# Optimization experiments

Hardware: AMD Instinct MI355X
Metric: run time of the kernel (lower is better)

## Reference

```python
import jax, jax.numpy as jnp
import numpy as np

SHAPE = (2048, 2048, 3, 3)  # conv kernel gradient [out_c, in_c, kh, kw]


def setup_inputs() -> dict:
    key = jax.random.key(0)
    k1, k2 = jax.random.split(key)
    grad = jax.random.normal(k1, SHAPE, dtype=jnp.float32)
    residual = jax.random.normal(k2, SHAPE, dtype=jnp.float32) * 0.1  # accumulated momentum residual self.layers[name]
    momentum = jnp.float32(0.9)
    k = int(np.prod(SHAPE) * 0.1 / 100)
    return {"grad": grad, "residual": residual, "momentum": momentum, "k": k}


def reference(grad, residual, momentum, k):
    # current_layer = tensor + self.layers[name], flattened
    flat = (grad + residual).reshape(-1)
    # top-k by absolute value
    _, idx_unsorted = jax.lax.top_k(jnp.abs(flat), k)
    vals_unsorted = flat[idx_unsorted]
    # sort selected entries by (signed) value, as torch.argsort(top_values_unsorted)
    order = jnp.argsort(vals_unsorted)
    top_values = vals_unsorted[order]
    top_indices = idx_unsorted[order]

    gflat = grad.reshape(-1)
    # small_values_tensor = grad with top entries zeroed (put_ with zeros)
    small = gflat.at[top_indices].set(0.0)
    # residual: zero top entries, then accumulate momentum-weighted small gradients
    new_residual = residual.reshape(-1).at[top_indices].set(0.0) + small * momentum
    # construct_grads: zeros with top values scattered at top_indices
    sparse_grad = jnp.zeros_like(gflat).at[top_indices].set(top_values)

    return (top_indices,
            top_values,
            new_residual.reshape(grad.shape),
            sparse_grad.reshape(grad.shape))
```

## Files before the change

kernel.cpp:

```cpp
#include <hip/hip_runtime.h>

typedef unsigned int u32;
typedef unsigned long long u64;

#define CAND_MAX 131072u
#define MEMB_MAX 65536u
#define SORT_N   65536u

__device__ __forceinline__ u32 fkey32(u32 fb) {
  return (fb & 0x80000000u) ? ~fb : (fb | 0x80000000u);
}

__global__ void k_hist(const float4* __restrict__ g, const float4* __restrict__ r,
                       int n4, u32* __restrict__ hist) {
  __shared__ u32 lh[2048];
  for (int i = threadIdx.x; i < 2048; i += blockDim.x) lh[i] = 0;
  __syncthreads();
  int stride = gridDim.x * blockDim.x;
  for (int i = blockIdx.x * blockDim.x + threadIdx.x; i < n4; i += stride) {
    float4 a = g[i]; float4 b = r[i];
    u32 u0 = __float_as_uint(a.x + b.x) & 0x7fffffffu;
    u32 u1 = __float_as_uint(a.y + b.y) & 0x7fffffffu;
    u32 u2 = __float_as_uint(a.z + b.z) & 0x7fffffffu;
    u32 u3 = __float_as_uint(a.w + b.w) & 0x7fffffffu;
    atomicAdd(&lh[u0 >> 20], 1u);
    atomicAdd(&lh[u1 >> 20], 1u);
    atomicAdd(&lh[u2 >> 20], 1u);
    atomicAdd(&lh[u3 >> 20], 1u);
  }
  __syncthreads();
  for (int i = threadIdx.x; i < 2048; i += blockDim.x)
    if (lh[i]) atomicAdd(&hist[i], lh[i]);
}

__global__ void __launch_bounds__(1024) k_scan(const u32* __restrict__ hist,
                                               u32* __restrict__ ctrl, int k) {
  __shared__ u32 b0[2048], b1[2048];
  u32 t = threadIdx.x;
  b0[t] = hist[t]; b0[t + 1024] = hist[t + 1024];
  __syncthreads();
  u32* src = b0; u32* dst = b1;
  for (u32 off = 1; off < 2048; off <<= 1) {
    for (u32 i = t; i < 2048; i += 1024) {
      u32 v = src[i];
      if (i + off < 2048) v += src[i + off];
      dst[i] = v;
    }
    __syncthreads();
    u32* tmp = src; src = dst; dst = tmp;
  }
  u32 K = (u32)k;
  for (u32 i = t; i < 2048; i += 1024) {
    u32 cum = src[i];
    u32 nxt = (i + 1 < 2048) ? src[i + 1] : 0u;
    if (cum >= K && nxt < K) {
      ctrl[0] = i;
      ctrl[1] = nxt;
      ctrl[2] = K - nxt;
    }
  }
}

__global__ void k_main(const float4* __restrict__ g, const float4* __restrict__ r,
                       const float* __restrict__ momp,
                       float4* __restrict__ res4, float4* __restrict__ sp4,
                       u32* __restrict__ ctrl, u64* __restrict__ cand,
                       u64* __restrict__ memb, int n4) {
  float m = *momp;
  u32 B = ctrl[0];
  int stride = gridDim.x * blockDim.x;
  for (int i = blockIdx.x * blockDim.x + threadIdx.x; i < n4; i += stride) {
    float4 a = g[i]; float4 b = r[i];
    float4 ro, so;
    u32 base = (u32)i * 4u;
#define PROC(X, J, RO, SO) { \
    float c = a.X + b.X; \
    u32 cb = __float_as_uint(c); \
    u32 u = cb & 0x7fffffffu; \
    u32 bin = u >> 20; \
    float rv = b.X + m * a.X; float sv = 0.f; \
    if (bin >= B) { \
      u32 idx = base + J; \
      if (bin > B) { \
        rv = 0.f; sv = c; \
        u32 slot = atomicAdd(&ctrl[4], 1u); \
        if (slot < MEMB_MAX) memb[slot] = ((u64)fkey32(cb) << 32) | (u64)idx; \
      } else { \
        u32 slot = atomicAdd(&ctrl[3], 1u); \
        if (slot < CAND_MAX) cand[slot] = ((u64)u << 32) | (u64)(idx | (cb & 0x80000000u)); \
      } \
    } \
    RO = rv; SO = sv; }
    PROC(x, 0u, ro.x, so.x)
    PROC(y, 1u, ro.y, so.y)
    PROC(z, 2u, ro.z, so.z)
    PROC(w, 3u, ro.w, so.w)
#undef PROC
    res4[i] = ro;
    sp4[i] = so;
  }
}

__global__ void __launch_bounds__(1024) k_refine(u32* __restrict__ ctrl,
                                                 const u64* __restrict__ cand) {
  __shared__ u32 h[1024], h2[1024];
  __shared__ u32 tie[2048];
  __shared__ u32 res[4];
  __shared__ u32 nt;
  u32 t = threadIdx.x;
  u32 nc = ctrl[3]; if (nc > CAND_MAX) nc = CAND_MAX;
  u32 r = ctrl[2];
  u32 B12 = ctrl[0];

  h[t] = 0; if (t == 0) nt = 0;
  __syncthreads();
  for (u32 i = t; i < nc; i += 1024) {
    u32 u = (u32)(cand[i] >> 32);
    atomicAdd(&h[(u >> 10) & 1023u], 1u);
  }
  __syncthreads();
  u32* src = h; u32* dst = h2;
  for (u32 off = 1; off < 1024; off <<= 1) {
    u32 v = src[t] + ((t + off < 1024) ? src[t + off] : 0u);
    dst[t] = v;
    __syncthreads();
    u32* tmp = src; src = dst; dst = tmp;
  }
  {
    u32 cum = src[t];
    u32 nxt = (t + 1 < 1024) ? src[t + 1] : 0u;
    if (cum >= r && nxt < r) { res[0] = t; res[1] = nxt; }
  }
  __syncthreads();
  u32 B1 = res[0];
  u32 r1 = r - res[1];
  __syncthreads();

  h[t] = 0; h2[t] = 0;
  __syncthreads();
  for (u32 i = t; i < nc; i += 1024) {
    u32 u = (u32)(cand[i] >> 32);
    if (((u >> 10) & 1023u) == B1) atomicAdd(&h[u & 1023u], 1u);
  }
  __syncthreads();
  src = h; dst = h2;
  for (u32 off = 1; off < 1024; off <<= 1) {
    u32 v = src[t] + ((t + off < 1024) ? src[t + off] : 0u);
    dst[t] = v;
    __syncthreads();
    u32* tmp = src; src = dst; dst = tmp;
  }
  {
    u32 cum = src[t];
    u32 nxt = (t + 1 < 1024) ? src[t + 1] : 0u;
    if (cum >= r1 && nxt < r1) { res[2] = t; res[3] = nxt; }
  }
  __syncthreads();
  u32 B2 = res[2];
  u32 r2 = r1 - res[3];
  u32 T = (B12 << 20) | (B1 << 10) | B2;
  __syncthreads();

  for (u32 i = t; i < nc; i += 1024) {
    u64 e = cand[i];
    if ((u32)(e >> 32) == T) {
      u32 p = atomicAdd(&nt, 1u);
      if (p < 2048u) tie[p] = (u32)e & 0x7fffffffu;
    }
  }
  __syncthreads();
  u32 ntc = nt; if (ntc > 2048u) ntc = 2048u;
  for (u32 i = t; i < ntc; i += 1024) {
    u32 ti = tie[i];
    u32 rank = 0;
    for (u32 j = 0; j < ntc; j++) rank += (tie[j] < ti) ? 1u : 0u;
    if (rank == r2 - 1u) ctrl[6] = ti;
  }
  if (t == 0) ctrl[5] = T;
}

__global__ void k_patch(u32* __restrict__ ctrl, const u64* __restrict__ cand,
                        float* __restrict__ res_out, float* __restrict__ sp_out,
                        u64* __restrict__ memb) {
  u32 nc = ctrl[3]; if (nc > CAND_MAX) nc = CAND_MAX;
  u32 T = ctrl[5];
  u32 cut = ctrl[6];
  u32 stride = gridDim.x * blockDim.x;
  for (u32 i = blockIdx.x * blockDim.x + threadIdx.x; i < nc; i += stride) {
    u64 e = cand[i];
    u32 u = (u32)(e >> 32);
    u32 low = (u32)e;
    u32 idx = low & 0x7fffffffu;
    bool chosen = (u > T) || (u == T && idx <= cut);
    if (chosen) {
      u32 cb = u | (low & 0x80000000u);
      res_out[idx] = 0.f;
      sp_out[idx] = __uint_as_float(cb);
      u32 slot = atomicAdd(&ctrl[4], 1u);
      if (slot < MEMB_MAX) memb[slot] = ((u64)fkey32(cb) << 32) | (u64)idx;
    }
  }
}

__global__ void k_pad(u64* __restrict__ memb, int k) {
  int i = blockIdx.x * blockDim.x + threadIdx.x;
  if (i >= k && i < (int)SORT_N) memb[i] = ~0ull;
}

__global__ void __launch_bounds__(1024) k_blocal(u64* __restrict__ d) {
  __shared__ u64 s[8192];
  u32 base = blockIdx.x * 8192u;
  for (u32 i = threadIdx.x; i < 8192u; i += blockDim.x) s[i] = d[base + i];
  __syncthreads();
  for (u32 kk = 2; kk <= 8192u; kk <<= 1) {
    for (u32 jj = kk >> 1; jj > 0; jj >>= 1) {
      for (u32 t = threadIdx.x; t < 4096u; t += blockDim.x) {
        u32 i = 2u * t - (t & (jj - 1u));
        u32 l = i + jj;
        u64 x = s[i], y = s[l];
        bool up = (((base + i) & kk) == 0u);
        bool sw = up ? (x > y) : (y > x);
        if (sw) { s[i] = y; s[l] = x; }
      }
      __syncthreads();
    }
  }
  for (u32 i = threadIdx.x; i < 8192u; i += blockDim.x) d[base + i] = s[i];
}

__global__ void __launch_bounds__(1024) k_bstep(u64* __restrict__ d, u32 kk, u32 jj) {
  u32 t = blockIdx.x * blockDim.x + threadIdx.x;
  u32 i = 2u * t - (t & (jj - 1u));
  u32 l = i + jj;
  u64 x = d[i], y = d[l];
  bool up = ((i & kk) == 0u);
  bool sw = up ? (x > y) : (y > x);
  if (sw) { d[i] = y; d[l] = x; }
}

__global__ void __launch_bounds__(1024) k_bmerge(u64* __restrict__ d, u32 kk) {
  __shared__ u64 s[8192];
  u32 base = blockIdx.x * 8192u;
  for (u32 i = threadIdx.x; i < 8192u; i += blockDim.x) s[i] = d[base + i];
  __syncthreads();
  for (u32 jj = 4096u; jj > 0; jj >>= 1) {
    for (u32 t = threadIdx.x; t < 4096u; t += blockDim.x) {
      u32 i = 2u * t - (t & (jj - 1u));
      u32 l = i + jj;
      u64 x = s[i], y = s[l];
      bool up = (((base + i) & kk) == 0u);
      bool sw = up ? (x > y) : (y > x);
      if (sw) { s[i] = y; s[l] = x; }
    }
    __syncthreads();
  }
  for (u32 i = threadIdx.x; i < 8192u; i += blockDim.x) d[base + i] = s[i];
}

__global__ void k_write(const u64* __restrict__ memb, float* __restrict__ out, int k) {
  int i = blockIdx.x * blockDim.x + threadIdx.x;
  if (i >= k) return;
  u64 e = memb[i];
  u32 idx = (u32)e;
  u32 h = (u32)(e >> 32);
  u32 fb = (h & 0x80000000u) ? (h ^ 0x80000000u) : ~h;
  out[i] = (float)idx;
  out[k + i] = __uint_as_float(fb);
}

extern "C" void kernel_launch(void* const* d_in, const int* in_sizes, int n_in,
                              void* d_out, int out_size, void* d_ws, size_t ws_size,
                              hipStream_t stream) {
  const float* g   = (const float*)d_in[0];
  const float* r   = (const float*)d_in[1];
  const float* mom = (const float*)d_in[2];
  int n = in_sizes[0];
  int k = (out_size - 2 * n) / 2;
  int n4 = n / 4;

  float* out = (float*)d_out;
  float* res_out = out + 2 * (size_t)k;
  float* sp_out  = res_out + (size_t)n;

  unsigned char* ws = (unsigned char*)d_ws;
  u32* hist = (u32*)ws;
  u32* ctrl = (u32*)(ws + 8192);
  u64* cand = (u64*)(ws + 16384);
  u64* memb = (u64*)(ws + 16384 + (size_t)CAND_MAX * 8);

  hipMemsetAsync(ws, 0, 16384, stream);

  k_hist<<<2048, 256, 0, stream>>>((const float4*)g, (const float4*)r, n4, hist);
  k_scan<<<1, 1024, 0, stream>>>(hist, ctrl, k);
  k_main<<<2048, 256, 0, stream>>>((const float4*)g, (const float4*)r, mom,
                                   (float4*)res_out, (float4*)sp_out,
                                   ctrl, cand, memb, n4);
  k_refine<<<1, 1024, 0, stream>>>(ctrl, cand);
  k_patch<<<256, 256, 0, stream>>>(ctrl, cand, res_out, sp_out, memb);
  k_pad<<<SORT_N / 256, 256, 0, stream>>>(memb, k);

  k_blocal<<<SORT_N / 8192, 1024, 0, stream>>>(memb);
  for (u32 kk = 16384u; kk <= SORT_N; kk <<= 1) {
    for (u32 jj = kk >> 1; jj >= 8192u; jj >>= 1)
      k_bstep<<<SORT_N / 2048, 1024, 0, stream>>>(memb, kk, jj);
    k_bmerge<<<SORT_N / 8192, 1024, 0, stream>>>(memb, kk);
  }

  k_write<<<(SORT_N + 255) / 256, 256, 0, stream>>>(memb, out, k);
}
```

Measured before the change: 1.160 ms.

## Replace full histogram pass with sampled threshold and wave-aggregated candidate append

Drops the full-tensor histogram pass and instead builds the coarse histogram from a sparse sample (1024 float4 per 32768 chunk), picking a looser threshold that targets about 4k candidates. The main pass writes only the residual and appends all above-threshold entries to the candidate list using wave-level ballot aggregation rather than per-element atomics. Refinement now does three histogram levels over the candidates, and the sparse output is zeroed with a memset. This removes one full read of both inputs and most global atomic contention. The cost is a larger candidate buffer, an extra refine level, a memset over the sparse output, and a dependence on the sample being representative: if the sample underestimates, fewer than k entries may fall above the threshold.

```diff
diff --git a/kernel.cpp b/kernel.cpp
--- a/kernel.cpp
+++ b/kernel.cpp
@@ -3,41 +3,66 @@
 typedef unsigned int u32;
 typedef unsigned long long u64;
 
-#define CAND_MAX 131072u
-#define MEMB_MAX 65536u
-#define SORT_N   65536u
+#define SORT_N 65536u
+
+#define C_PT    0
+#define C_NC    16
+#define C_T     32
+#define C_CUT   33
+#define C_NM    48
 
 __device__ __forceinline__ u32 fkey32(u32 fb) {
   return (fb & 0x80000000u) ? ~fb : (fb | 0x80000000u);
 }
 
-__global__ void k_hist(const float4* __restrict__ g, const float4* __restrict__ r,
-                       int n4, u32* __restrict__ hist) {
+__device__ __forceinline__ u32 lane_id() {
+  return __builtin_amdgcn_mbcnt_hi(~0u, __builtin_amdgcn_mbcnt_lo(~0u, 0u));
+}
+
+__device__ __forceinline__ u32 wave_append(u32* ctr, bool pred) {
+  u64 mask = __ballot(pred);
+  if (mask == 0ull) return 0xffffffffu;
+  u32 lane = lane_id();
+  u32 slot = 0xffffffffu;
+  if (pred) {
+    u32 rank = (u32)__popcll(mask & ((1ull << lane) - 1ull));
+    int leader = __ffsll((unsigned long long)mask) - 1;
+    u32 base = 0;
+    if ((int)lane == leader) base = atomicAdd(ctr, (u32)__popcll(mask));
+    base = (u32)__shfl((int)base, leader, 64);
+    slot = base + rank;
+  }
+  return slot;
+}
+
+__global__ void __launch_bounds__(256) k_sample(const float4* __restrict__ g,
+                                                const float4* __restrict__ r,
+                                                u32* __restrict__ shist, int n4) {
   __shared__ u32 lh[2048];
-  for (int i = threadIdx.x; i < 2048; i += blockDim.x) lh[i] = 0;
-  __syncthreads();
-  int stride = gridDim.x * blockDim.x;
-  for (int i = blockIdx.x * blockDim.x + threadIdx.x; i < n4; i += stride) {
-    float4 a = g[i]; float4 b = r[i];
-    u32 u0 = __float_as_uint(a.x + b.x) & 0x7fffffffu;
-    u32 u1 = __float_as_uint(a.y + b.y) & 0x7fffffffu;
-    u32 u2 = __float_as_uint(a.z + b.z) & 0x7fffffffu;
-    u32 u3 = __float_as_uint(a.w + b.w) & 0x7fffffffu;
-    atomicAdd(&lh[u0 >> 20], 1u);
-    atomicAdd(&lh[u1 >> 20], 1u);
-    atomicAdd(&lh[u2 >> 20], 1u);
-    atomicAdd(&lh[u3 >> 20], 1u);
-  }
-  __syncthreads();
-  for (int i = threadIdx.x; i < 2048; i += blockDim.x)
-    if (lh[i]) atomicAdd(&hist[i], lh[i]);
-}
-
-__global__ void __launch_bounds__(1024) k_scan(const u32* __restrict__ hist,
-                                               u32* __restrict__ ctrl, int k) {
+  for (int i = threadIdx.x; i < 2048; i += 256) lh[i] = 0;
+  __syncthreads();
+  u32 base = blockIdx.x * 32768u;
+#pragma unroll
+  for (int j = 0; j < 4; j++) {
+    u32 i = base + threadIdx.x + (u32)j * 256u;
+    if ((int)i < n4) {
+      float4 a = g[i]; float4 b = r[i];
+      atomicAdd(&lh[(__float_as_uint(a.x + b.x) & 0x7fffffffu) >> 20], 1u);
+      atomicAdd(&lh[(__float_as_uint(a.y + b.y) & 0x7fffffffu) >> 20], 1u);
+      atomicAdd(&lh[(__float_as_uint(a.z + b.z) & 0x7fffffffu) >> 20], 1u);
+      atomicAdd(&lh[(__float_as_uint(a.w + b.w) & 0x7fffffffu) >> 20], 1u);
+    }
+  }
+  __syncthreads();
+  for (int i = threadIdx.x; i < 2048; i += 256)
+    if (lh[i]) atomicAdd(&shist[i], lh[i]);
+}
+
+__global__ void __launch_bounds__(1024) k_pick(const u32* __restrict__ shist,
+                                               u32* __restrict__ ctrl, u32 target) {
   __shared__ u32 b0[2048], b1[2048];
   u32 t = threadIdx.x;
-  b0[t] = hist[t]; b0[t + 1024] = hist[t + 1024];
+  b0[t] = shist[t]; b0[t + 1024] = shist[t + 1024];
   __syncthreads();
   u32* src = b0; u32* dst = b1;
   for (u32 off = 1; off < 2048; off <<= 1) {
@@ -49,79 +74,93 @@
     __syncthreads();
     u32* tmp = src; src = dst; dst = tmp;
   }
-  u32 K = (u32)k;
   for (u32 i = t; i < 2048; i += 1024) {
     u32 cum = src[i];
     u32 nxt = (i + 1 < 2048) ? src[i + 1] : 0u;
-    if (cum >= K && nxt < K) {
-      ctrl[0] = i;
-      ctrl[1] = nxt;
-      ctrl[2] = K - nxt;
-    }
-  }
-}
-
-__global__ void k_main(const float4* __restrict__ g, const float4* __restrict__ r,
-                       const float* __restrict__ momp,
-                       float4* __restrict__ res4, float4* __restrict__ sp4,
-                       u32* __restrict__ ctrl, u64* __restrict__ cand,
-                       u64* __restrict__ memb, int n4) {
-  float m = *momp;
-  u32 B = ctrl[0];
-  int stride = gridDim.x * blockDim.x;
-  for (int i = blockIdx.x * blockDim.x + threadIdx.x; i < n4; i += stride) {
-    float4 a = g[i]; float4 b = r[i];
-    float4 ro, so;
-    u32 base = (u32)i * 4u;
-#define PROC(X, J, RO, SO) { \
-    float c = a.X + b.X; \
-    u32 cb = __float_as_uint(c); \
+    if (cum >= target && nxt < target) ctrl[C_PT] = i;
+  }
+}
+
+__global__ void __launch_bounds__(256) k_main1(const float4* __restrict__ g,
+                                               const float4* __restrict__ r,
+                                               const float* __restrict__ momp,
+                                               float4* __restrict__ res4,
+                                               u32* __restrict__ ctrl,
+                                               u64* __restrict__ cand, u32 cap, int n4) {
+  int i = blockIdx.x * 256 + (int)threadIdx.x;
+  if (i >= n4) return;
+  float m = momp[0];
+  u32 PT = ctrl[C_PT];
+  float4 a = g[i];
+  float4 b = r[i];
+  float4 ro;
+  ro.x = b.x + m * a.x; ro.y = b.y + m * a.y;
+  ro.z = b.z + m * a.z; ro.w = b.w + m * a.w;
+  res4[i] = ro;
+  u32 base4 = (u32)i * 4u;
+  float cv0 = a.x + b.x, cv1 = a.y + b.y, cv2 = a.z + b.z, cv3 = a.w + b.w;
+#define COMPACT(CV, J) { \
+    u32 cb = __float_as_uint(CV); \
     u32 u = cb & 0x7fffffffu; \
-    u32 bin = u >> 20; \
-    float rv = b.X + m * a.X; float sv = 0.f; \
-    if (bin >= B) { \
-      u32 idx = base + J; \
-      if (bin > B) { \
-        rv = 0.f; sv = c; \
-        u32 slot = atomicAdd(&ctrl[4], 1u); \
-        if (slot < MEMB_MAX) memb[slot] = ((u64)fkey32(cb) << 32) | (u64)idx; \
-      } else { \
-        u32 slot = atomicAdd(&ctrl[3], 1u); \
-        if (slot < CAND_MAX) cand[slot] = ((u64)u << 32) | (u64)(idx | (cb & 0x80000000u)); \
-      } \
-    } \
-    RO = rv; SO = sv; }
-    PROC(x, 0u, ro.x, so.x)
-    PROC(y, 1u, ro.y, so.y)
-    PROC(z, 2u, ro.z, so.z)
-    PROC(w, 3u, ro.w, so.w)
-#undef PROC
-    res4[i] = ro;
-    sp4[i] = so;
-  }
+    bool pred = (u >> 20) >= PT; \
+    u32 slot = wave_append(&ctrl[C_NC], pred); \
+    if (pred && slot < cap) \
+      cand[slot] = ((u64)u << 32) | (u64)((base4 + J) | (cb & 0x80000000u)); \
+  }
+  COMPACT(cv0, 0u)
+  COMPACT(cv1, 1u)
+  COMPACT(cv2, 2u)
+  COMPACT(cv3, 3u)
+#undef COMPACT
 }
 
 __global__ void __launch_bounds__(1024) k_refine(u32* __restrict__ ctrl,
-                                                 const u64* __restrict__ cand) {
-  __shared__ u32 h[1024], h2[1024];
+                                                 const u64* __restrict__ cand,
+                                                 u32 cap, u32 K) {
+  __shared__ u32 h[2048], h2[2048];
+  __shared__ u32 res[8];
   __shared__ u32 tie[2048];
-  __shared__ u32 res[4];
   __shared__ u32 nt;
   u32 t = threadIdx.x;
-  u32 nc = ctrl[3]; if (nc > CAND_MAX) nc = CAND_MAX;
-  u32 r = ctrl[2];
-  u32 B12 = ctrl[0];
-
-  h[t] = 0; if (t == 0) nt = 0;
+  u32 nc = ctrl[C_NC]; if (nc > cap) nc = cap;
+
+  h[t] = 0; h[t + 1024] = 0;
+  if (t == 0) nt = 0;
+  __syncthreads();
+  for (u32 i = t; i < nc; i += 1024)
+    atomicAdd(&h[(u32)(cand[i] >> 52)], 1u);
+  __syncthreads();
+  u32* src = h; u32* dst = h2;
+  for (u32 off = 1; off < 2048; off <<= 1) {
+    for (u32 i = t; i < 2048; i += 1024) {
+      u32 v = src[i];
+      if (i + off < 2048) v += src[i + off];
+      dst[i] = v;
+    }
+    __syncthreads();
+    u32* tmp = src; src = dst; dst = tmp;
+  }
+  for (u32 i = t; i < 2048; i += 1024) {
+    u32 cum = src[i];
+    u32 nxt = (i + 1 < 2048) ? src[i + 1] : 0u;
+    if (cum >= K && nxt < K) { res[0] = i; res[1] = nxt; }
+  }
+  __syncthreads();
+  u32 B0 = res[0];
+  u32 r0 = K - res[1];
+  __syncthreads();
+
+  h[t] = 0;
   __syncthreads();
   for (u32 i = t; i < nc; i += 1024) {
     u32 u = (u32)(cand[i] >> 32);
-    atomicAdd(&h[(u >> 10) & 1023u], 1u);
-  }
-  __syncthreads();
-  u32* src = h; u32* dst = h2;
+    if ((u >> 20) == B0) atomicAdd(&h[(u >> 10) & 1023u], 1u);
+  }
+  __syncthreads();
+  src = h; dst = h2;
   for (u32 off = 1; off < 1024; off <<= 1) {
-    u32 v = src[t] + ((t + off < 1024) ? src[t + off] : 0u);
+    u32 v = src[t];
+    if (t + off < 1024) v += src[t + off];
     dst[t] = v;
     __syncthreads();
     u32* tmp = src; src = dst; dst = tmp;
@@ -129,23 +168,25 @@
   {
     u32 cum = src[t];
     u32 nxt = (t + 1 < 1024) ? src[t + 1] : 0u;
-    if (cum >= r && nxt < r) { res[0] = t; res[1] = nxt; }
-  }
-  __syncthreads();
-  u32 B1 = res[0];
-  u32 r1 = r - res[1];
-  __syncthreads();
-
-  h[t] = 0; h2[t] = 0;
+    if (cum >= r0 && nxt < r0) { res[2] = t; res[3] = nxt; }
+  }
+  __syncthreads();
+  u32 B1 = res[2];
+  u32 r1 = r0 - res[3];
+  u32 hi21 = (B0 << 10) | B1;
+  __syncthreads();
+
+  h[t] = 0;
   __syncthreads();
   for (u32 i = t; i < nc; i += 1024) {
     u32 u = (u32)(cand[i] >> 32);
-    if (((u >> 10) & 1023u) == B1) atomicAdd(&h[u & 1023u], 1u);
+    if ((u >> 10) == hi21) atomicAdd(&h[u & 1023u], 1u);
   }
   __syncthreads();
   src = h; dst = h2;
   for (u32 off = 1; off < 1024; off <<= 1) {
-    u32 v = src[t] + ((t + off < 1024) ? src[t + off] : 0u);
+    u32 v = src[t];
+    if (t + off < 1024) v += src[t + off];
     dst[t] = v;
     __syncthreads();
     u32* tmp = src; src = dst; dst = tmp;
@@ -153,12 +194,12 @@
   {
     u32 cum = src[t];
     u32 nxt = (t + 1 < 1024) ? src[t + 1] : 0u;
-    if (cum >= r1 && nxt < r1) { res[2] = t; res[3] = nxt; }
-  }
-  __syncthreads();
-  u32 B2 = res[2];
-  u32 r2 = r1 - res[3];
-  u32 T = (B12 << 20) | (B1 << 10) | B2;
+    if (cum >= r1 && nxt < r1) { res[4] = t; res[5] = nxt; }
+  }
+  __syncthreads();
+  u32 B2 = res[4];
+  u32 r2 = r1 - res[5];
+  u32 T = (hi21 << 10) | B2;
   __syncthreads();
 
   for (u32 i = t; i < nc; i += 1024) {
@@ -174,30 +215,38 @@
     u32 ti = tie[i];
     u32 rank = 0;
     for (u32 j = 0; j < ntc; j++) rank += (tie[j] < ti) ? 1u : 0u;
-    if (rank == r2 - 1u) ctrl[6] = ti;
-  }
-  if (t == 0) ctrl[5] = T;
-}
-
-__global__ void k_patch(u32* __restrict__ ctrl, const u64* __restrict__ cand,
-                        float* __restrict__ res_out, float* __restrict__ sp_out,
-                        u64* __restrict__ memb) {
-  u32 nc = ctrl[3]; if (nc > CAND_MAX) nc = CAND_MAX;
-  u32 T = ctrl[5];
-  u32 cut = ctrl[6];
-  u32 stride = gridDim.x * blockDim.x;
-  for (u32 i = blockIdx.x * blockDim.x + threadIdx.x; i < nc; i += stride) {
-    u64 e = cand[i];
-    u32 u = (u32)(e >> 32);
-    u32 low = (u32)e;
-    u32 idx = low & 0x7fffffffu;
-    bool chosen = (u > T) || (u == T && idx <= cut);
+    if (rank == r2 - 1u) ctrl[C_CUT] = ti;
+  }
+  if (t == 0) ctrl[C_T] = T;
+}
+
+__global__ void __launch_bounds__(256) k_patch(u32* __restrict__ ctrl,
+                                               const u64* __restrict__ cand, u32 cap,
+                                               float* __restrict__ res_out,
+                                               float* __restrict__ sp_out,
+                                               u64* __restrict__ memb) {
+  u32 nc = ctrl[C_NC]; if (nc > cap) nc = cap;
+  u32 T = ctrl[C_T];
+  u32 cut = ctrl[C_CUT];
+  u32 total = gridDim.x * blockDim.x;
+  u32 iters = (cap + total - 1u) / total;
+  u32 i = blockIdx.x * blockDim.x + threadIdx.x;
+  for (u32 it = 0; it < iters; it++, i += total) {
+    bool chosen = false;
+    u32 idx = 0, cb = 0;
+    if (i < nc) {
+      u64 e = cand[i];
+      u32 u = (u32)(e >> 32);
+      u32 low = (u32)e;
+      idx = low & 0x7fffffffu;
+      cb = u | (low & 0x80000000u);
+      chosen = (u > T) || (u == T && idx <= cut);
+    }
+    u32 slot = wave_append(&ctrl[C_NM], chosen);
     if (chosen) {
-      u32 cb = u | (low & 0x80000000u);
       res_out[idx] = 0.f;
       sp_out[idx] = __uint_as_float(cb);
-      u32 slot = atomicAdd(&ctrl[4], 1u);
-      if (slot < MEMB_MAX) memb[slot] = ((u64)fkey32(cb) << 32) | (u64)idx;
+      memb[slot] = ((u64)fkey32(cb) << 32) | (u64)idx;
     }
   }
 }
@@ -261,7 +310,7 @@
   int i = blockIdx.x * blockDim.x + threadIdx.x;
   if (i >= k) return;
   u64 e = memb[i];
-  u32 idx = (u32)e;
+  u32 idx = (u32)e & 0x7fffffffu;
   u32 h = (u32)(e >> 32);
   u32 fb = (h & 0x80000000u) ? (h ^ 0x80000000u) : ~h;
   out[i] = (float)idx;
@@ -283,20 +332,33 @@
   float* sp_out  = res_out + (size_t)n;
 
   unsigned char* ws = (unsigned char*)d_ws;
-  u32* hist = (u32*)ws;
-  u32* ctrl = (u32*)(ws + 8192);
-  u64* cand = (u64*)(ws + 16384);
-  u64* memb = (u64*)(ws + 16384 + (size_t)CAND_MAX * 8);
+  u32* ctrl  = (u32*)ws;
+  u32* shist = (u32*)(ws + 1024);
+  u64* memb  = (u64*)(ws + 16384);
+  size_t cand_off = 16384 + (size_t)SORT_N * 8;
+  u64* cand  = (u64*)(ws + cand_off);
+
+  u32 cap = 2097152u;
+  if (ws_size < cand_off + (size_t)cap * 8)
+    cap = (u32)((ws_size - cand_off) / 8);
+
+  int nsc = n4 / 32768; if (nsc < 1) nsc = 1;
+  double sampleN = (double)nsc * 1024.0 * 4.0;
+  double want = 4.0 * (double)k;
+  double capd = 0.6 * (double)cap;
+  if (want > capd) want = capd;
+  if (want < 1.5 * (double)k) want = 1.5 * (double)k;
+  u32 target = (u32)(want * sampleN / (double)n) + 1u;
 
   hipMemsetAsync(ws, 0, 16384, stream);
-
-  k_hist<<<2048, 256, 0, stream>>>((const float4*)g, (const float4*)r, n4, hist);
-  k_scan<<<1, 1024, 0, stream>>>(hist, ctrl, k);
-  k_main<<<2048, 256, 0, stream>>>((const float4*)g, (const float4*)r, mom,
-                                   (float4*)res_out, (float4*)sp_out,
-                                   ctrl, cand, memb, n4);
-  k_refine<<<1, 1024, 0, stream>>>(ctrl, cand);
-  k_patch<<<256, 256, 0, stream>>>(ctrl, cand, res_out, sp_out, memb);
+  hipMemsetAsync(sp_out, 0, (size_t)n * sizeof(float), stream);
+
+  k_sample<<<nsc, 256, 0, stream>>>((const float4*)g, (const float4*)r, shist, n4);
+  k_pick<<<1, 1024, 0, stream>>>(shist, ctrl, target);
+  k_main1<<<(n4 + 255) / 256, 256, 0, stream>>>((const float4*)g, (const float4*)r, mom,
+                                                (float4*)res_out, ctrl, cand, cap, n4);
+  k_refine<<<1, 1024, 0, stream>>>(ctrl, cand, cap, (u32)k);
+  k_patch<<<2048, 256, 0, stream>>>(ctrl, cand, cap, res_out, sp_out, memb);
   k_pad<<<SORT_N / 256, 256, 0, stream>>>(memb, k);
 
   k_blocal<<<SORT_N / 8192, 1024, 0, stream>>>(memb);
```

Measured after the change: 3.020 ms. +160.4%, slower.
